# Performance work log

Measured on AMD Instinct MI355X. Metric: run time of the kernel, lower is better.

Reference implementation:

```python
import jax, jax.numpy as jnp
import numpy as np

NEG_INF = -9e15
ALPHA = 0.2  # leaky_relu slope


def gat_layer(h, adj, e_feat, W, We, a_s, a_d, a_e, h_res):
    """Dense multi-head GAT layer with edge features.
    h: [B,N,Fin], adj: [B,N,N] (0/1), e_feat: [B,N,N,Ein]
    W: [H,Fin,Fout], We: [H,Ein,Eout], a_s/a_d: [H,Fout], a_e: [H,Eout]
    Returns head-averaged (x_prime [B,N,Fout], e_prime [B,N,N,Eout]).
    """
    Wh = jnp.einsum('bnf,hfo->bhno', h, W)            # [B,H,N,Fout]
    Me = jnp.einsum('bnmf,hfe->bhnme', e_feat, We)    # [B,H,N,N,Eout]
    s_src = jnp.einsum('bhno,ho->bhn', Wh, a_s)
    s_dst = jnp.einsum('bhno,ho->bhn', Wh, a_d)
    s_edge = jnp.einsum('bhnme,he->bhnm', Me, a_e)
    scores = jax.nn.leaky_relu(s_src[:, :, :, None] + s_dst[:, :, None, :] + s_edge, ALPHA)
    scores = jnp.where(adj[:, None, :, :] > 0, scores, NEG_INF)
    att = jax.nn.softmax(scores, axis=-1)             # [B,H,N,N]
    h_prime = jnp.einsum('bhnm,bhmo->bhno', att, Wh)
    h_prime = jax.nn.elu(h_prime) + h_res[:, None]    # concat=True -> elu; residual add
    e_prime = att[..., None] * Me                      # attention-modulated edge features
    return h_prime.mean(axis=1), e_prime.mean(axis=1)


def setup_inputs() -> dict:
    key = jax.random.key(0)
    ks = jax.random.split(key, 16)
    B, N, F, E, H = 2, 256, 768, 7, 2
    nhid, ehid = 768, 768 // 2
    sc = lambda fan: 1.0 / np.sqrt(fan)
    return {
        'x': jax.random.normal(ks[0], (B, N, F), jnp.float32),
        'adj': jax.random.randint(ks[1], (B, N, N), 0, 2, jnp.int32),
        'e': jax.random.uniform(ks[2], (B, N, N, E), jnp.float32),
        'W1': jax.random.normal(ks[3], (H, F, nhid), jnp.float32) * sc(F),
        'We1': jax.random.normal(ks[4], (H, E, ehid), jnp.float32) * sc(E),
        'a1s': jax.random.normal(ks[5], (H, nhid), jnp.float32) * sc(nhid),
        'a1d': jax.random.normal(ks[6], (H, nhid), jnp.float32) * sc(nhid),
        'a1e': jax.random.normal(ks[7], (H, ehid), jnp.float32) * sc(ehid),
        'W2': jax.random.normal(ks[8], (H, nhid, nhid), jnp.float32) * sc(nhid),
        'We2': jax.random.normal(ks[9], (H, ehid, ehid), jnp.float32) * sc(ehid),
        'a2s': jax.random.normal(ks[10], (H, nhid), jnp.float32) * sc(nhid),
        'a2d': jax.random.normal(ks[11], (H, nhid), jnp.float32) * sc(nhid),
        'a2e': jax.random.normal(ks[12], (H, ehid), jnp.float32) * sc(ehid),
    }


def reference(x, adj, e, W1, We1, a1s, a1d, a1e, W2, We2, a2s, a2d, a2e):
    # dropout layers are identity in eval mode
    x1, e1 = gat_layer(x, adj, e, W1, We1, a1s, a1d, a1e, x)
    x2, e2 = gat_layer(x1, adj, e1, W2, We2, a2s, a2d, a2e, x)
    return x2, e2
```

## Files before the change

kernel.cpp:

```cpp
#include <hip/hip_runtime.h>
#include <hip/hip_bf16.h>
#include <cstddef>


typedef __attribute__((ext_vector_type(8))) short bf16x8;
typedef __attribute__((ext_vector_type(4))) short bf16x4;
typedef __attribute__((ext_vector_type(4))) float f32x4;
typedef unsigned short us;

#define DEVINL static __device__ __forceinline__

DEVINL us f2bf(float f) {
    union { float f; unsigned u; } v; v.f = f;
    return (us)((v.u + 0x7FFFu + ((v.u >> 16) & 1u)) >> 16);
}
DEVINL float bf2f(us b) {
    union { unsigned u; float f; } v; v.u = ((unsigned)b) << 16; return v.f;
}
DEVINL float wredmax(float v) {
#pragma unroll
    for (int s = 32; s; s >>= 1) v = fmaxf(v, __shfl_xor(v, s));
    return v;
}
DEVINL float wredsum(float v) {
#pragma unroll
    for (int s = 32; s; s >>= 1) v += __shfl_xor(v, s);
    return v;
}

DEVINL void transpose_body(const float* __restrict__ W, us* __restrict__ WT, int bb) {
    __shared__ us tile[64][65];
    const int ft = (bb % 12) * 64, ot = ((bb / 12) % 12) * 64, h = bb / 144;
    const int t = threadIdx.x;
    const float* Wh = W + (size_t)h * 768 * 768;
    us* WTh = WT + (size_t)h * 768 * 768;
#pragma unroll
    for (int i = 0; i < 16; i++) {
        int idx = t + i * 256, r = idx >> 6, c = idx & 63;
        tile[c][r] = f2bf(Wh[(ft + r) * 768 + ot + c]);
    }
    __syncthreads();
#pragma unroll
    for (int i = 0; i < 2; i++) {
        int idx = t + i * 256, r = idx >> 3, c0 = (idx & 7) * 8;
        us pk[8];
#pragma unroll
        for (int j = 0; j < 8; j++) pk[j] = tile[r][c0 + j];
        *(bf16x8*)&WTh[(ot + r) * 768 + ft + c0] = *(bf16x8*)pk;
    }
}

DEVINL void cvt_body(const float* __restrict__ in, us* __restrict__ out, int blk) {
    int i = (blk * 256 + threadIdx.x) * 8;
    float4 v0 = *(const float4*)&in[i];
    float4 v1 = *(const float4*)&in[i + 4];
    us pk[8] = {f2bf(v0.x), f2bf(v0.y), f2bf(v0.z), f2bf(v0.w),
                f2bf(v1.x), f2bf(v1.y), f2bf(v1.z), f2bf(v1.w)};
    *(bf16x8*)&out[i] = *(bf16x8*)pk;
}

DEVINL void pre_body(const float* __restrict__ W1, const float* __restrict__ W2,
                     const float* __restrict__ We1, const float* __restrict__ We2,
                     const float* __restrict__ a1s, const float* __restrict__ a1d,
                     const float* __restrict__ a1e, const float* __restrict__ a2s,
                     const float* __restrict__ a2d,
                     float* __restrict__ q, float* __restrict__ u1,
                     float* __restrict__ Mcat, int blk) {
    const int g = blk * 32 + (threadIdx.x >> 3);
    const int lane = threadIdx.x & 7;
    float acc = 0.0f;
    if (g < 6144) {
        int vec = g / 1536, rem = g % 1536, h = rem / 768, f = rem % 768;
        const float* W = (vec < 2) ? W1 : W2;
        const float* a = (vec == 0) ? a1s : (vec == 1) ? a1d : (vec == 2) ? a2s : a2d;
        const float* wr = W + (size_t)(h * 768 + f) * 768;
        const float* ar = a + h * 768;
        for (int o = lane; o < 768; o += 8) acc += wr[o] * ar[o];
        for (int s = 4; s; s >>= 1) acc += __shfl_down(acc, s, 8);
        if (lane == 0) q[g] = acc;
    } else if (g < 6160) {
        int g2 = g - 6144, h = g2 >> 3, k = g2 & 7;
        if (k < 7) {
            const float* wr = We1 + (h * 7 + k) * 384;
            const float* ar = a1e + h * 384;
            for (int o = lane; o < 384; o += 8) acc += wr[o] * ar[o];
        }
        for (int s = 4; s; s >>= 1) acc += __shfl_down(acc, s, 8);
        if (lane == 0) u1[g2] = acc;
    } else if (g < 18448) {
        int g3 = g - 6160, rk = g3 / 384, tc = g3 % 384;
        int hh = rk >> 3, kk = rk & 7, h1 = hh >> 1, h2 = hh & 1;
        if (kk < 7) {
            const float* wr = We1 + (h1 * 7 + kk) * 384;
            const float* w2c = We2 + (size_t)h2 * 384 * 384 + tc;
            for (int o = lane; o < 384; o += 8) acc += wr[o] * w2c[o * 384];
            acc *= 0.25f;
        }
        for (int s = 4; s; s >>= 1) acc += __shfl_down(acc, s, 8);
        if (lane == 0) Mcat[g3] = acc;
    }
}

DEVINL void wcalc_body(const float* __restrict__ Mcat, const float* __restrict__ a2e,
                       float* __restrict__ w) {
    const int t = threadIdx.x, g = t >> 3, lane = t & 7;
    int hh = g >> 3, k = g & 7, h2 = hh & 1;
    float acc = 0.0f;
    if (k < 7)
        for (int o = lane; o < 384; o += 8) acc += Mcat[(hh * 8 + k) * 384 + o] * a2e[h2 * 384 + o];
    for (int s = 4; s; s >>= 1) acc += __shfl_down(acc, s, 8);
    if (lane == 0) w[g] = 2.0f * acc;
}

DEVINL void bfrag_body(const float* __restrict__ Mcat, us* __restrict__ Bfrag, int ct) {
    const int l = threadIdx.x;
    if (l < 64) {
        us pk[8];
#pragma unroll
        for (int j = 0; j < 8; j++)
            pk[j] = f2bf(Mcat[((l >> 4) * 8 + j) * 384 + ct * 16 + (l & 15)]);
        *(bf16x8*)&Bfrag[(ct * 64 + l) * 8] = *(bf16x8*)pk;
    }
}

DEVINL void sdots_body(const float* __restrict__ x, const float* __restrict__ qs,
                       const float* __restrict__ qd, float* __restrict__ out_s,
                       float* __restrict__ out_d, int n, int b) {
    const int t = threadIdx.x, wv = t >> 6;
    const float* xr = x + (size_t)(b * 256 + n) * 768;
    float a0 = 0, a1 = 0, a2 = 0, a3 = 0;
#pragma unroll
    for (int i = 0; i < 3; i++) {
        int k = i * 256 + t;
        float xv = xr[k];
        a0 += xv * qs[k];
        a1 += xv * qs[768 + k];
        a2 += xv * qd[k];
        a3 += xv * qd[768 + k];
    }
    a0 = wredsum(a0); a1 = wredsum(a1); a2 = wredsum(a2); a3 = wredsum(a3);
    __shared__ float part[4][4];
    if ((t & 63) == 0) { part[wv][0] = a0; part[wv][1] = a1; part[wv][2] = a2; part[wv][3] = a3; }
    __syncthreads();
    if (t == 0) {
        float r0 = 0, r1 = 0, r2 = 0, r3 = 0;
#pragma unroll
        for (int i = 0; i < 4; i++) { r0 += part[i][0]; r1 += part[i][1]; r2 += part[i][2]; r3 += part[i][3]; }
        out_s[(b * 2 + 0) * 256 + n] = r0;
        out_s[(b * 2 + 1) * 256 + n] = r1;
        out_d[(b * 2 + 0) * 256 + n] = r2;
        out_d[(b * 2 + 1) * 256 + n] = r3;
    }
}

DEVINL void att_finish2(float sc0, float sc1, us* __restrict__ attb,
                        size_t base0, size_t base1) {
    const int t = threadIdx.x, wv = t >> 6;
    __shared__ float smax[2][4], ssum[2][4];
    float w0 = wredmax(sc0), w1 = wredmax(sc1);
    if ((t & 63) == 0) { smax[0][wv] = w0; smax[1][wv] = w1; }
    __syncthreads();
    float mx0 = fmaxf(fmaxf(smax[0][0], smax[0][1]), fmaxf(smax[0][2], smax[0][3]));
    float mx1 = fmaxf(fmaxf(smax[1][0], smax[1][1]), fmaxf(smax[1][2], smax[1][3]));
    float ex0 = __expf(sc0 - mx0), ex1 = __expf(sc1 - mx1);
    float su0 = wredsum(ex0), su1 = wredsum(ex1);
    if ((t & 63) == 0) { ssum[0][wv] = su0; ssum[1][wv] = su1; }
    __syncthreads();
    float i0 = 1.0f / (ssum[0][0] + ssum[0][1] + ssum[0][2] + ssum[0][3]);
    float i1 = 1.0f / (ssum[1][0] + ssum[1][1] + ssum[1][2] + ssum[1][3]);
    attb[base0 + t] = f2bf(ex0 * i0);
    attb[base1 + t] = f2bf(ex1 * i1);
}

DEVINL void att1_body(const float* __restrict__ e, const int* __restrict__ adj,
                      const float* __restrict__ s_s, const float* __restrict__ s_d,
                      const float* __restrict__ u1, us* __restrict__ attb,
                      int n, int bb) {
    __shared__ float eL[1792];
    const int t = threadIdx.x;
    const float* erow = e + (size_t)(bb * 256 + n) * 256 * 7;
#pragma unroll
    for (int i = 0; i < 7; i++) eL[t + i * 256] = erow[t + i * 256];
    __syncthreads();
    float ss0 = s_s[(bb * 2 + 0) * 256 + n], ss1 = s_s[(bb * 2 + 1) * 256 + n];
    float sd0 = s_d[(bb * 2 + 0) * 256 + t], sd1 = s_d[(bb * 2 + 1) * 256 + t];
    float se0 = 0, se1 = 0;
#pragma unroll
    for (int k = 0; k < 7; k++) {
        float ev = eL[t * 7 + k];
        se0 += ev * u1[k];
        se1 += ev * u1[8 + k];
    }
    float sc0 = ss0 + sd0 + se0, sc1 = ss1 + sd1 + se1;
    sc0 = sc0 > 0.0f ? sc0 : 0.2f * sc0;
    sc1 = sc1 > 0.0f ? sc1 : 0.2f * sc1;
    bool ok = adj[(size_t)(bb * 256 + n) * 256 + t] > 0;
    sc0 = ok ? sc0 : -9e15f;
    sc1 = ok ? sc1 : -9e15f;
    size_t base0 = ((size_t)(bb * 2 + 0) * 256 + n) * 256;
    size_t base1 = ((size_t)(bb * 2 + 1) * 256 + n) * 256;
    att_finish2(sc0, sc1, attb, base0, base1);
}

DEVINL void att2_body(const float* __restrict__ e, const int* __restrict__ adj,
                      const float* __restrict__ s_s, const float* __restrict__ s_d,
                      const float* __restrict__ w, const us* __restrict__ att1b,
                      us* __restrict__ attb, int n, int bb) {
    __shared__ float eL[1792];
    const int t = threadIdx.x;
    const float* erow = e + (size_t)(bb * 256 + n) * 256 * 7;
#pragma unroll
    for (int i = 0; i < 7; i++) eL[t + i * 256] = erow[t + i * 256];
    __syncthreads();
    float ss0 = s_s[(bb * 2 + 0) * 256 + n], ss1 = s_s[(bb * 2 + 1) * 256 + n];
    float sd0 = s_d[(bb * 2 + 0) * 256 + t], sd1 = s_d[(bb * 2 + 1) * 256 + t];
    float a10 = bf2f(att1b[((size_t)(bb * 2 + 0) * 256 + n) * 256 + t]);
    float a11 = bf2f(att1b[((size_t)(bb * 2 + 1) * 256 + n) * 256 + t]);
    float ew00 = 0, ew01 = 0, ew10 = 0, ew11 = 0;
#pragma unroll
    for (int k = 0; k < 7; k++) {
        float ev = eL[t * 7 + k];
        ew00 += ev * w[0 * 8 + k];
        ew01 += ev * w[1 * 8 + k];
        ew10 += ev * w[2 * 8 + k];
        ew11 += ev * w[3 * 8 + k];
    }
    float sc0 = ss0 + sd0 + a10 * ew00 + a11 * ew10;
    float sc1 = ss1 + sd1 + a10 * ew01 + a11 * ew11;
    sc0 = sc0 > 0.0f ? sc0 : 0.2f * sc0;
    sc1 = sc1 > 0.0f ? sc1 : 0.2f * sc1;
    bool ok = adj[(size_t)(bb * 256 + n) * 256 + t] > 0;
    sc0 = ok ? sc0 : -9e15f;
    sc1 = ok ? sc1 : -9e15f;
    size_t base0 = ((size_t)(bb * 2 + 0) * 256 + n) * 256;
    size_t base1 = ((size_t)(bb * 2 + 1) * 256 + n) * 256;
    att_finish2(sc0, sc1, attb, base0, base1);
}

DEVINL void gemm_xw_body(const us* __restrict__ A, const us* __restrict__ BT,
                         us* __restrict__ WhT, int mt, int ot, int h) {
    const int t = threadIdx.x, wv = t >> 6, l = t & 63;
    const int wm = wv >> 1, wn = wv & 1, lr = l & 15, lk = l >> 4;
    __shared__ us As[64][40];
    __shared__ us Bs[64][40];
    const int arow = t >> 2, acol = (t & 3) * 8;
    const us* Bh = BT + (size_t)h * 768 * 768;
    f32x4 acc[2][2];
#pragma unroll
    for (int i = 0; i < 2; i++)
#pragma unroll
        for (int j = 0; j < 2; j++) acc[i][j] = (f32x4){0, 0, 0, 0};
    for (int k0 = 0; k0 < 768; k0 += 32) {
        __syncthreads();
        *(bf16x8*)&As[arow][acol] = *(const bf16x8*)&A[(size_t)(mt * 64 + arow) * 768 + k0 + acol];
        *(bf16x8*)&Bs[arow][acol] = *(const bf16x8*)&Bh[(size_t)(ot * 64 + arow) * 768 + k0 + acol];
        __syncthreads();
        bf16x8 af[2], bfv[2];
#pragma unroll
        for (int i = 0; i < 2; i++) af[i] = *(const bf16x8*)&As[wm * 32 + i * 16 + lr][lk * 8];
#pragma unroll
        for (int j = 0; j < 2; j++) bfv[j] = *(const bf16x8*)&Bs[wn * 32 + j * 16 + lr][lk * 8];
#pragma unroll
        for (int i = 0; i < 2; i++)
#pragma unroll
            for (int j = 0; j < 2; j++)
                acc[i][j] = __builtin_amdgcn_mfma_f32_16x16x32_bf16(af[i], bfv[j], acc[i][j], 0, 0, 0);
    }
#pragma unroll
    for (int i = 0; i < 2; i++)
#pragma unroll
        for (int j = 0; j < 2; j++) {
            int n0 = mt * 64 + wm * 32 + i * 16 + lk * 4;
            int og = ot * 64 + wn * 32 + j * 16 + lr;
            int b = n0 >> 8, n = n0 & 255;
            us pk[4];
#pragma unroll
            for (int r = 0; r < 4; r++) pk[r] = f2bf(acc[i][j][r]);
            *(bf16x4*)&WhT[((size_t)(b * 2 + h) * 768 + og) * 256 + n] = *(bf16x4*)pk;
        }
}

DEVINL void gemm_att_body(const us* __restrict__ attb, const us* __restrict__ WhT,
                          const float* __restrict__ resid, float* __restrict__ xout,
                          us* __restrict__ xbout, int mt, int ot, int b) {
    const int t = threadIdx.x, wv = t >> 6, l = t & 63;
    const int wm = wv >> 1, wn = wv & 1, lr = l & 15, lk = l >> 4;
    __shared__ us As2[32][40];
    __shared__ us Bs2[64][40];
    float res[2][4] = {};
    for (int h = 0; h < 2; h++) {
        const us* Ah = attb + (size_t)(b * 2 + h) * 65536;
        const us* Bh = WhT + (size_t)(b * 2 + h) * 768 * 256;
        f32x4 acc[2];
        acc[0] = (f32x4){0, 0, 0, 0};
        acc[1] = (f32x4){0, 0, 0, 0};
        for (int k0 = 0; k0 < 256; k0 += 32) {
            __syncthreads();
            if (t < 128) {
                int ar = t >> 2, ac = (t & 3) * 8;
                *(bf16x8*)&As2[ar][ac] = *(const bf16x8*)&Ah[(size_t)(mt * 32 + ar) * 256 + k0 + ac];
            }
            {
                int br = t >> 2, bc = (t & 3) * 8;
                *(bf16x8*)&Bs2[br][bc] = *(const bf16x8*)&Bh[(size_t)(ot * 64 + br) * 256 + k0 + bc];
            }
            __syncthreads();
            bf16x8 af = *(const bf16x8*)&As2[wm * 16 + lr][lk * 8];
#pragma unroll
            for (int j = 0; j < 2; j++) {
                bf16x8 bv = *(const bf16x8*)&Bs2[wn * 32 + j * 16 + lr][lk * 8];
                acc[j] = __builtin_amdgcn_mfma_f32_16x16x32_bf16(af, bv, acc[j], 0, 0, 0);
            }
        }
#pragma unroll
        for (int j = 0; j < 2; j++)
#pragma unroll
            for (int r = 0; r < 4; r++) {
                float v = acc[j][r];
                res[j][r] += (v > 0.0f ? v : (expf(v) - 1.0f));
            }
        __syncthreads();
    }
#pragma unroll
    for (int j = 0; j < 2; j++) {
        int n0 = mt * 32 + wm * 16 + lk * 4;
        int og = ot * 64 + wn * 32 + j * 16 + lr;
#pragma unroll
        for (int r = 0; r < 4; r++) {
            size_t idx = (size_t)(b * 256 + n0 + r) * 768 + og;
            float v = 0.5f * res[j][r] + resid[idx];
            xout[idx] = v;
            if (xbout) xbout[idx] = f2bf(v);
        }
    }
}

DEVINL void e2row_body(const float* __restrict__ e, const us* __restrict__ att1b,
                       const us* __restrict__ att2b, const us* __restrict__ Bfrag,
                       float* __restrict__ e2out, int bb, int n) {
    __shared__ us blB[1536 * 8];
    __shared__ float eL[1792];
    __shared__ float aL[4][256];
    const int t = threadIdx.x;
    for (int i = t; i < 1536; i += 256)
        *(bf16x8*)&blB[i * 8] = *(const bf16x8*)&Bfrag[(size_t)i * 8];
    const float* erow = e + (size_t)(bb * 256 + n) * 256 * 7;
#pragma unroll
    for (int i = 0; i < 7; i++) eL[t + i * 256] = erow[t + i * 256];
    const size_t abase = (size_t)bb * 2 * 65536 + n * 256;
    aL[0][t] = bf2f(att1b[abase + t]);
    aL[1][t] = bf2f(att1b[abase + 65536 + t]);
    aL[2][t] = bf2f(att2b[abase + t]);
    aL[3][t] = bf2f(att2b[abase + 65536 + t]);
    __syncthreads();
    const int wv = t >> 6, l = t & 63, le = l & 15, lq = l >> 4;
    const int h1 = lq >> 1, h2 = lq & 1;
    bf16x8 av[4];
#pragma unroll
    for (int g = 0; g < 4; g++) {
        int m = g * 64 + wv * 16 + le;
        float c = aL[h1][m] * aL[2 + h2][m];
        us pk[8];
#pragma unroll
        for (int j = 0; j < 7; j++) pk[j] = f2bf(c * eL[m * 7 + j]);
        pk[7] = 0;
        av[g] = *(bf16x8*)pk;
    }
    const f32x4 zero = {0, 0, 0, 0};
    const size_t rowbase = (size_t)bb * 65536 + n * 256;
#pragma unroll
    for (int cg = 0; cg < 3; cg++) {
        bf16x8 bfr[8];
#pragma unroll
        for (int i = 0; i < 8; i++) bfr[i] = *(const bf16x8*)&blB[(cg * 512 + i * 64 + l) * 8];
        for (int g = 0; g < 4; g++) {
            size_t eidx = rowbase + g * 64 + wv * 16 + le;
#pragma unroll
            for (int i = 0; i < 8; i++) {
                f32x4 acc = __builtin_amdgcn_mfma_f32_16x16x32_bf16(bfr[i], av[g], zero, 0, 0, 0);
                *(f32x4*)&e2out[eidx * 384 + cg * 128 + i * 16 + lq * 4] = acc;
            }
        }
    }
}

__global__ __launch_bounds__(256) void stage1(
    const float* W1, const float* W2, const float* We1, const float* We2,
    const float* a1s, const float* a1d, const float* a1e,
    const float* a2s, const float* a2d,
    const float* x, us* W1T, us* W2T, us* xb,
    float* q, float* u1, float* Mcat) {
    int b = blockIdx.x;
    if (b < 577)       pre_body(W1, W2, We1, We2, a1s, a1d, a1e, a2s, a2d, q, u1, Mcat, b);
    else if (b < 865)  transpose_body(W1, W1T, b - 577);
    else if (b < 1153) transpose_body(W2, W2T, b - 865);
    else               cvt_body(x, xb, b - 1153);
}

__global__ __launch_bounds__(256) void stage2(
    const float* Mcat, const float* a2e, float* wbuf, us* Bfrag,
    const float* x, const float* qs, const float* qd, float* s1s, float* s1d) {
    int b = blockIdx.x;
    if (b < 1)        wcalc_body(Mcat, a2e, wbuf);
    else if (b < 25)  bfrag_body(Mcat, Bfrag, b - 1);
    else { int i = b - 25; sdots_body(x, qs, qd, s1s, s1d, i & 255, i >> 8); }
}

__global__ __launch_bounds__(256) void stage3(
    const float* e, const int* adj, const float* s1s, const float* s1d,
    const float* u1, us* att1b, const us* xb, const us* W1T, us* WhT1) {
    int b = blockIdx.x;
    if (b < 512) att1_body(e, adj, s1s, s1d, u1, att1b, b & 255, b >> 8);
    else { int g = b - 512; gemm_xw_body(xb, W1T, WhT1, g & 7, (g >> 3) % 12, g / 96); }
}

__global__ __launch_bounds__(256) void stage4(
    const us* att1b, const us* WhT1, const float* x, float* x1, us* xb1) {
    int b = blockIdx.x;
    gemm_att_body(att1b, WhT1, x, x1, xb1, b & 7, (b >> 3) % 12, b / 96);
}

__global__ __launch_bounds__(256) void stage5(
    const float* x1, const float* qs, const float* qd, float* s2s, float* s2d,
    const us* xb1, const us* W2T, us* WhT2) {
    int b = blockIdx.x;
    if (b < 512) sdots_body(x1, qs, qd, s2s, s2d, b & 255, b >> 8);
    else { int g = b - 512; gemm_xw_body(xb1, W2T, WhT2, g & 7, (g >> 3) % 12, g / 96); }
}

__global__ __launch_bounds__(256) void stage6(
    const float* e, const int* adj, const float* s2s, const float* s2d,
    const float* wbuf, const us* att1b, us* att2b) {
    int b = blockIdx.x;
    att2_body(e, adj, s2s, s2d, wbuf, att1b, att2b, b & 255, b >> 8);
}

__global__ __launch_bounds__(256) void stage7(
    const us* att2b, const us* WhT2, const float* x, float* x2out,
    const float* e, const us* att1b, const us* Bfrag, float* e2out) {
    int b = blockIdx.x;
    if (b < 192) gemm_att_body(att2b, WhT2, x, x2out, (us*)nullptr, b & 7, (b >> 3) % 12, b / 96);
    else { int r = b - 192; e2row_body(e, att1b, att2b, Bfrag, e2out, r >> 8, r & 255); }
}

extern "C" void kernel_launch(void* const* d_in, const int* in_sizes, int n_in,
                              void* d_out, int out_size, void* d_ws, size_t ws_size,
                              hipStream_t stream) {
    const float* x   = (const float*)d_in[0];
    const int*   adj = (const int*)d_in[1];
    const float* e   = (const float*)d_in[2];
    const float* W1  = (const float*)d_in[3];
    const float* We1 = (const float*)d_in[4];
    const float* a1s = (const float*)d_in[5];
    const float* a1d = (const float*)d_in[6];
    const float* a1e = (const float*)d_in[7];
    const float* W2  = (const float*)d_in[8];
    const float* We2 = (const float*)d_in[9];
    const float* a2s = (const float*)d_in[10];
    const float* a2d = (const float*)d_in[11];
    const float* a2e = (const float*)d_in[12];

    float* out   = (float*)d_out;
    float* x2out = out;
    float* e2out = out + 393216;

    char* ws = (char*)d_ws;
    float* q     = (float*)(ws + 0);
    float* u1    = (float*)(ws + 24576);
    float* wbuf  = (float*)(ws + 24640);
    float* Mcat  = (float*)(ws + 24832);
    us*    Bfrag = (us*)(ws + 73984);
    float* s1s   = (float*)(ws + 98560);
    float* s1d   = (float*)(ws + 102656);
    float* s2s   = (float*)(ws + 106752);
    float* s2d   = (float*)(ws + 110848);
    us*    att1b = (us*)(ws + 114944);
    us*    att2b = (us*)(ws + 639232);
    us*    W1T   = (us*)(ws + 1163520);
    us*    W2T   = (us*)(ws + 3522816);
    us*    xb    = (us*)(ws + 5882112);
    us*    xb1   = (us*)(ws + 6668544);
    us*    WhT1  = (us*)(ws + 7454976);
    us*    WhT2  = (us*)(ws + 9027840);
    float* x1    = (float*)(ws + 10600704);

    stage1<<<1345, 256, 0, stream>>>(W1, W2, We1, We2, a1s, a1d, a1e, a2s, a2d,
                                     x, W1T, W2T, xb, q, u1, Mcat);
    stage2<<<537, 256, 0, stream>>>(Mcat, a2e, wbuf, Bfrag, x, q + 0, q + 1536, s1s, s1d);
    stage3<<<704, 256, 0, stream>>>(e, adj, s1s, s1d, u1, att1b, xb, W1T, WhT1);
    stage4<<<192, 256, 0, stream>>>(att1b, WhT1, x, x1, xb1);
    stage5<<<704, 256, 0, stream>>>(x1, q + 3072, q + 4608, s2s, s2d, xb1, W2T, WhT2);
    stage6<<<512, 256, 0, stream>>>(e, adj, s2s, s2d, wbuf, att1b, att2b);
    stage7<<<704, 256, 0, stream>>>(att2b, WhT2, x, x2out, e, att1b, Bfrag, e2out);
}
```

Baseline: 106.0 us.

## Fuse score dots into GEMM epilogues and merge attention-2 with edge output

The q vectors (W·a) are now computed inside the W transpose blocks using wave reductions and atomics, replacing the separate pre_body pass. The second layer's source and destination score dots are accumulated in the stage4 GEMM epilogue through shared and global atomics, so the x1 fp32 buffer and the sdots stage go away. Attention-2 softmax is fused with the e2 output computation in one block, and Mcat gets a shared-memory tiled kernel. Together these cut the launch count from 7 to 6 and remove extra passes over memory, at the cost of atomics, two memsets, and a summation order that is no longer deterministic.

```diff
diff --git a/kernel.cpp b/kernel.cpp
--- a/kernel.cpp
+++ b/kernel.cpp
@@ -28,16 +28,27 @@
     return v;
 }
 
-DEVINL void transpose_body(const float* __restrict__ W, us* __restrict__ WT, int bb) {
+DEVINL void transposeq_body(const float* __restrict__ W, us* __restrict__ WT,
+                            const float* __restrict__ as_, const float* __restrict__ ad_,
+                            float* __restrict__ q, int qbase, int bb) {
     __shared__ us tile[64][65];
     const int ft = (bb % 12) * 64, ot = ((bb / 12) % 12) * 64, h = bb / 144;
-    const int t = threadIdx.x;
-    const float* Wh = W + (size_t)h * 768 * 768;
-    us* WTh = WT + (size_t)h * 768 * 768;
+    const int t = threadIdx.x, c = t & 63, g = t >> 6;
+    const float* Wh = W + (size_t)h * 589824;
+    us* WTh = WT + (size_t)h * 589824;
+    const float avs = as_[h * 768 + ot + c];
+    const float avd = ad_[h * 768 + ot + c];
 #pragma unroll
     for (int i = 0; i < 16; i++) {
-        int idx = t + i * 256, r = idx >> 6, c = idx & 63;
-        tile[c][r] = f2bf(Wh[(ft + r) * 768 + ot + c]);
+        int r = g + i * 4;
+        float w = Wh[(size_t)(ft + r) * 768 + ot + c];
+        tile[c][r] = f2bf(w);
+        float ss = wredsum(w * avs);
+        float sd = wredsum(w * avd);
+        if (c == 0) {
+            atomicAdd(&q[qbase + h * 768 + ft + r], ss);
+            atomicAdd(&q[qbase + 1536 + h * 768 + ft + r], sd);
+        }
     }
     __syncthreads();
 #pragma unroll
@@ -46,7 +57,56 @@
         us pk[8];
 #pragma unroll
         for (int j = 0; j < 8; j++) pk[j] = tile[r][c0 + j];
-        *(bf16x8*)&WTh[(ot + r) * 768 + ft + c0] = *(bf16x8*)pk;
+        *(bf16x8*)&WTh[(size_t)(ot + r) * 768 + ft + c0] = *(bf16x8*)pk;
+    }
+}
+
+DEVINL void mcat_body(const float* __restrict__ We1, const float* __restrict__ We2,
+                      float* __restrict__ Mcat, int h2, int tct) {
+    __shared__ float we1L[16][384];
+    __shared__ float part[16][128];
+    const int t = threadIdx.x;
+    for (int i = t; i < 6144; i += 256) {
+        int m = i / 384, o = i % 384;
+        int h1 = m >> 3, kk = m & 7;
+        we1L[m][o] = (kk < 7) ? We1[(h1 * 7 + kk) * 384 + o] : 0.0f;
+    }
+    __syncthreads();
+    const int tc = tct * 128 + (t & 127);
+    const int half = t >> 7;
+    float acc[16];
+#pragma unroll
+    for (int m = 0; m < 16; m++) acc[m] = 0.0f;
+    const float* w2 = We2 + (size_t)h2 * 147456 + tc;
+    for (int o = half * 192; o < half * 192 + 192; o++) {
+        float wv = w2[(size_t)o * 384];
+#pragma unroll
+        for (int m = 0; m < 16; m++) acc[m] += we1L[m][o] * wv;
+    }
+    if (half == 1)
+#pragma unroll
+        for (int m = 0; m < 16; m++) part[m][t & 127] = acc[m];
+    __syncthreads();
+    if (half == 0) {
+#pragma unroll
+        for (int m = 0; m < 16; m++) {
+            float v = 0.25f * (acc[m] + part[m][t]);
+            int h1 = m >> 3, kk = m & 7;
+            Mcat[((h1 * 2 + h2) * 8 + kk) * 384 + tc] = v;
+        }
+    }
+}
+
+DEVINL void u1_body(const float* __restrict__ We1, const float* __restrict__ a1e,
+                    float* __restrict__ u1) {
+    const int t = threadIdx.x, g = t >> 4, lane = t & 15;
+    if (g < 14) {
+        int h = g / 7, k = g % 7;
+        float acc = 0.0f;
+        for (int o = lane; o < 384; o += 16) acc += We1[(h * 7 + k) * 384 + o] * a1e[h * 384 + o];
+#pragma unroll
+        for (int s = 8; s; s >>= 1) acc += __shfl_xor(acc, s, 16);
+        if (lane == 0) u1[h * 8 + k] = acc;
     }
 }
 
@@ -57,48 +117,6 @@
     us pk[8] = {f2bf(v0.x), f2bf(v0.y), f2bf(v0.z), f2bf(v0.w),
                 f2bf(v1.x), f2bf(v1.y), f2bf(v1.z), f2bf(v1.w)};
     *(bf16x8*)&out[i] = *(bf16x8*)pk;
-}
-
-DEVINL void pre_body(const float* __restrict__ W1, const float* __restrict__ W2,
-                     const float* __restrict__ We1, const float* __restrict__ We2,
-                     const float* __restrict__ a1s, const float* __restrict__ a1d,
-                     const float* __restrict__ a1e, const float* __restrict__ a2s,
-                     const float* __restrict__ a2d,
-                     float* __restrict__ q, float* __restrict__ u1,
-                     float* __restrict__ Mcat, int blk) {
-    const int g = blk * 32 + (threadIdx.x >> 3);
-    const int lane = threadIdx.x & 7;
-    float acc = 0.0f;
-    if (g < 6144) {
-        int vec = g / 1536, rem = g % 1536, h = rem / 768, f = rem % 768;
-        const float* W = (vec < 2) ? W1 : W2;
-        const float* a = (vec == 0) ? a1s : (vec == 1) ? a1d : (vec == 2) ? a2s : a2d;
-        const float* wr = W + (size_t)(h * 768 + f) * 768;
-        const float* ar = a + h * 768;
-        for (int o = lane; o < 768; o += 8) acc += wr[o] * ar[o];
-        for (int s = 4; s; s >>= 1) acc += __shfl_down(acc, s, 8);
-        if (lane == 0) q[g] = acc;
-    } else if (g < 6160) {
-        int g2 = g - 6144, h = g2 >> 3, k = g2 & 7;
-        if (k < 7) {
-            const float* wr = We1 + (h * 7 + k) * 384;
-            const float* ar = a1e + h * 384;
-            for (int o = lane; o < 384; o += 8) acc += wr[o] * ar[o];
-        }
-        for (int s = 4; s; s >>= 1) acc += __shfl_down(acc, s, 8);
-        if (lane == 0) u1[g2] = acc;
-    } else if (g < 18448) {
-        int g3 = g - 6160, rk = g3 / 384, tc = g3 % 384;
-        int hh = rk >> 3, kk = rk & 7, h1 = hh >> 1, h2 = hh & 1;
-        if (kk < 7) {
-            const float* wr = We1 + (h1 * 7 + kk) * 384;
-            const float* w2c = We2 + (size_t)h2 * 384 * 384 + tc;
-            for (int o = lane; o < 384; o += 8) acc += wr[o] * w2c[o * 384];
-            acc *= 0.25f;
-        }
-        for (int s = 4; s; s >>= 1) acc += __shfl_down(acc, s, 8);
-        if (lane == 0) Mcat[g3] = acc;
-    }
 }
 
 DEVINL void wcalc_body(const float* __restrict__ Mcat, const float* __restrict__ a2e,
@@ -153,32 +171,14 @@
     }
 }
 
-DEVINL void att_finish2(float sc0, float sc1, us* __restrict__ attb,
-                        size_t base0, size_t base1) {
-    const int t = threadIdx.x, wv = t >> 6;
-    __shared__ float smax[2][4], ssum[2][4];
-    float w0 = wredmax(sc0), w1 = wredmax(sc1);
-    if ((t & 63) == 0) { smax[0][wv] = w0; smax[1][wv] = w1; }
-    __syncthreads();
-    float mx0 = fmaxf(fmaxf(smax[0][0], smax[0][1]), fmaxf(smax[0][2], smax[0][3]));
-    float mx1 = fmaxf(fmaxf(smax[1][0], smax[1][1]), fmaxf(smax[1][2], smax[1][3]));
-    float ex0 = __expf(sc0 - mx0), ex1 = __expf(sc1 - mx1);
-    float su0 = wredsum(ex0), su1 = wredsum(ex1);
-    if ((t & 63) == 0) { ssum[0][wv] = su0; ssum[1][wv] = su1; }
-    __syncthreads();
-    float i0 = 1.0f / (ssum[0][0] + ssum[0][1] + ssum[0][2] + ssum[0][3]);
-    float i1 = 1.0f / (ssum[1][0] + ssum[1][1] + ssum[1][2] + ssum[1][3]);
-    attb[base0 + t] = f2bf(ex0 * i0);
-    attb[base1 + t] = f2bf(ex1 * i1);
-}
-
 DEVINL void att1_body(const float* __restrict__ e, const int* __restrict__ adj,
                       const float* __restrict__ s_s, const float* __restrict__ s_d,
                       const float* __restrict__ u1, us* __restrict__ attb,
                       int n, int bb) {
     __shared__ float eL[1792];
-    const int t = threadIdx.x;
-    const float* erow = e + (size_t)(bb * 256 + n) * 256 * 7;
+    __shared__ float smax[2][4], ssum[2][4];
+    const int t = threadIdx.x, wv = t >> 6;
+    const float* erow = e + (size_t)(bb * 256 + n) * 1792;
 #pragma unroll
     for (int i = 0; i < 7; i++) eL[t + i * 256] = erow[t + i * 256];
     __syncthreads();
@@ -197,44 +197,19 @@
     bool ok = adj[(size_t)(bb * 256 + n) * 256 + t] > 0;
     sc0 = ok ? sc0 : -9e15f;
     sc1 = ok ? sc1 : -9e15f;
-    size_t base0 = ((size_t)(bb * 2 + 0) * 256 + n) * 256;
-    size_t base1 = ((size_t)(bb * 2 + 1) * 256 + n) * 256;
-    att_finish2(sc0, sc1, attb, base0, base1);
-}
-
-DEVINL void att2_body(const float* __restrict__ e, const int* __restrict__ adj,
-                      const float* __restrict__ s_s, const float* __restrict__ s_d,
-                      const float* __restrict__ w, const us* __restrict__ att1b,
-                      us* __restrict__ attb, int n, int bb) {
-    __shared__ float eL[1792];
-    const int t = threadIdx.x;
-    const float* erow = e + (size_t)(bb * 256 + n) * 256 * 7;
-#pragma unroll
-    for (int i = 0; i < 7; i++) eL[t + i * 256] = erow[t + i * 256];
-    __syncthreads();
-    float ss0 = s_s[(bb * 2 + 0) * 256 + n], ss1 = s_s[(bb * 2 + 1) * 256 + n];
-    float sd0 = s_d[(bb * 2 + 0) * 256 + t], sd1 = s_d[(bb * 2 + 1) * 256 + t];
-    float a10 = bf2f(att1b[((size_t)(bb * 2 + 0) * 256 + n) * 256 + t]);
-    float a11 = bf2f(att1b[((size_t)(bb * 2 + 1) * 256 + n) * 256 + t]);
-    float ew00 = 0, ew01 = 0, ew10 = 0, ew11 = 0;
-#pragma unroll
-    for (int k = 0; k < 7; k++) {
-        float ev = eL[t * 7 + k];
-        ew00 += ev * w[0 * 8 + k];
-        ew01 += ev * w[1 * 8 + k];
-        ew10 += ev * w[2 * 8 + k];
-        ew11 += ev * w[3 * 8 + k];
-    }
-    float sc0 = ss0 + sd0 + a10 * ew00 + a11 * ew10;
-    float sc1 = ss1 + sd1 + a10 * ew01 + a11 * ew11;
-    sc0 = sc0 > 0.0f ? sc0 : 0.2f * sc0;
-    sc1 = sc1 > 0.0f ? sc1 : 0.2f * sc1;
-    bool ok = adj[(size_t)(bb * 256 + n) * 256 + t] > 0;
-    sc0 = ok ? sc0 : -9e15f;
-    sc1 = ok ? sc1 : -9e15f;
-    size_t base0 = ((size_t)(bb * 2 + 0) * 256 + n) * 256;
-    size_t base1 = ((size_t)(bb * 2 + 1) * 256 + n) * 256;
-    att_finish2(sc0, sc1, attb, base0, base1);
+    float w0 = wredmax(sc0), w1 = wredmax(sc1);
+    if ((t & 63) == 0) { smax[0][wv] = w0; smax[1][wv] = w1; }
+    __syncthreads();
+    float mx0 = fmaxf(fmaxf(smax[0][0], smax[0][1]), fmaxf(smax[0][2], smax[0][3]));
+    float mx1 = fmaxf(fmaxf(smax[1][0], smax[1][1]), fmaxf(smax[1][2], smax[1][3]));
+    float ex0 = __expf(sc0 - mx0), ex1 = __expf(sc1 - mx1);
+    float su0 = wredsum(ex0), su1 = wredsum(ex1);
+    if ((t & 63) == 0) { ssum[0][wv] = su0; ssum[1][wv] = su1; }
+    __syncthreads();
+    float i0 = 1.0f / (ssum[0][0] + ssum[0][1] + ssum[0][2] + ssum[0][3]);
+    float i1 = 1.0f / (ssum[1][0] + ssum[1][1] + ssum[1][2] + ssum[1][3]);
+    attb[((size_t)(bb * 2 + 0) * 256 + n) * 256 + t] = f2bf(ex0 * i0);
+    attb[((size_t)(bb * 2 + 1) * 256 + n) * 256 + t] = f2bf(ex1 * i1);
 }
 
 DEVINL void gemm_xw_body(const us* __restrict__ A, const us* __restrict__ BT,
@@ -244,7 +219,7 @@
     __shared__ us As[64][40];
     __shared__ us Bs[64][40];
     const int arow = t >> 2, acol = (t & 3) * 8;
-    const us* Bh = BT + (size_t)h * 768 * 768;
+    const us* Bh = BT + (size_t)h * 589824;
     f32x4 acc[2][2];
 #pragma unroll
     for (int i = 0; i < 2; i++)
@@ -282,15 +257,19 @@
 
 DEVINL void gemm_att_body(const us* __restrict__ attb, const us* __restrict__ WhT,
                           const float* __restrict__ resid, float* __restrict__ xout,
-                          us* __restrict__ xbout, int mt, int ot, int b) {
+                          us* __restrict__ xbout, const float* __restrict__ q,
+                          float* __restrict__ s2s, float* __restrict__ s2d,
+                          int mt, int ot, int b) {
     const int t = threadIdx.x, wv = t >> 6, l = t & 63;
     const int wm = wv >> 1, wn = wv & 1, lr = l & 15, lk = l >> 4;
     __shared__ us As2[32][40];
     __shared__ us Bs2[64][40];
+    __shared__ float sAcc[4][32];
+    if (s2s && t < 128) ((float*)sAcc)[t] = 0.0f;
     float res[2][4] = {};
     for (int h = 0; h < 2; h++) {
         const us* Ah = attb + (size_t)(b * 2 + h) * 65536;
-        const us* Bh = WhT + (size_t)(b * 2 + h) * 768 * 256;
+        const us* Bh = WhT + (size_t)(b * 2 + h) * 196608;
         f32x4 acc[2];
         acc[0] = (f32x4){0, 0, 0, 0};
         acc[1] = (f32x4){0, 0, 0, 0};
@@ -325,33 +304,94 @@
     for (int j = 0; j < 2; j++) {
         int n0 = mt * 32 + wm * 16 + lk * 4;
         int og = ot * 64 + wn * 32 + j * 16 + lr;
+        float qs0 = 0, qs1 = 0, qd0 = 0, qd1 = 0;
+        if (s2s) {
+            qs0 = q[3072 + og]; qs1 = q[3072 + 768 + og];
+            qd0 = q[4608 + og]; qd1 = q[4608 + 768 + og];
+        }
 #pragma unroll
         for (int r = 0; r < 4; r++) {
             size_t idx = (size_t)(b * 256 + n0 + r) * 768 + og;
             float v = 0.5f * res[j][r] + resid[idx];
-            xout[idx] = v;
+            if (xout) xout[idx] = v;
             if (xbout) xbout[idx] = f2bf(v);
-        }
-    }
-}
-
-DEVINL void e2row_body(const float* __restrict__ e, const us* __restrict__ att1b,
-                       const us* __restrict__ att2b, const us* __restrict__ Bfrag,
-                       float* __restrict__ e2out, int bb, int n) {
+            if (s2s) {
+                int row = wm * 16 + lk * 4 + r;
+                atomicAdd(&sAcc[0][row], v * qs0);
+                atomicAdd(&sAcc[1][row], v * qs1);
+                atomicAdd(&sAcc[2][row], v * qd0);
+                atomicAdd(&sAcc[3][row], v * qd1);
+            }
+        }
+    }
+    if (s2s) {
+        __syncthreads();
+        if (t < 128) {
+            int type = t >> 5, row = t & 31, n = mt * 32 + row;
+            float* dst = (type == 0) ? &s2s[(b * 2 + 0) * 256 + n]
+                       : (type == 1) ? &s2s[(b * 2 + 1) * 256 + n]
+                       : (type == 2) ? &s2d[(b * 2 + 0) * 256 + n]
+                                     : &s2d[(b * 2 + 1) * 256 + n];
+            atomicAdd(dst, sAcc[type][row]);
+        }
+    }
+}
+
+DEVINL void att2e2_body(const float* __restrict__ e, const int* __restrict__ adj,
+                        const float* __restrict__ s_s, const float* __restrict__ s_d,
+                        const float* __restrict__ w, const us* __restrict__ att1b,
+                        us* __restrict__ att2b, const us* __restrict__ Bfrag,
+                        float* __restrict__ e2out, int bb, int n) {
     __shared__ us blB[1536 * 8];
     __shared__ float eL[1792];
-    __shared__ float aL[4][256];
-    const int t = threadIdx.x;
+    __shared__ float aL1[2][256], aL2[2][256];
+    __shared__ float smax[2][4], ssum[2][4];
+    const int t = threadIdx.x, wv4 = t >> 6;
     for (int i = t; i < 1536; i += 256)
         *(bf16x8*)&blB[i * 8] = *(const bf16x8*)&Bfrag[(size_t)i * 8];
-    const float* erow = e + (size_t)(bb * 256 + n) * 256 * 7;
+    const float* erow = e + (size_t)(bb * 256 + n) * 1792;
 #pragma unroll
     for (int i = 0; i < 7; i++) eL[t + i * 256] = erow[t + i * 256];
-    const size_t abase = (size_t)bb * 2 * 65536 + n * 256;
-    aL[0][t] = bf2f(att1b[abase + t]);
-    aL[1][t] = bf2f(att1b[abase + 65536 + t]);
-    aL[2][t] = bf2f(att2b[abase + t]);
-    aL[3][t] = bf2f(att2b[abase + 65536 + t]);
+    const size_t a1base = (size_t)bb * 131072 + n * 256;
+    float a10 = bf2f(att1b[a1base + t]);
+    float a11 = bf2f(att1b[a1base + 65536 + t]);
+    aL1[0][t] = a10;
+    aL1[1][t] = a11;
+    __syncthreads();
+    float ss0 = s_s[(bb * 2 + 0) * 256 + n], ss1 = s_s[(bb * 2 + 1) * 256 + n];
+    float sd0 = s_d[(bb * 2 + 0) * 256 + t], sd1 = s_d[(bb * 2 + 1) * 256 + t];
+    float ew00 = 0, ew01 = 0, ew10 = 0, ew11 = 0;
+#pragma unroll
+    for (int k = 0; k < 7; k++) {
+        float ev = eL[t * 7 + k];
+        ew00 += ev * w[k];
+        ew01 += ev * w[8 + k];
+        ew10 += ev * w[16 + k];
+        ew11 += ev * w[24 + k];
+    }
+    float sc0 = ss0 + sd0 + a10 * ew00 + a11 * ew10;
+    float sc1 = ss1 + sd1 + a10 * ew01 + a11 * ew11;
+    sc0 = sc0 > 0.0f ? sc0 : 0.2f * sc0;
+    sc1 = sc1 > 0.0f ? sc1 : 0.2f * sc1;
+    bool ok = adj[(size_t)(bb * 256 + n) * 256 + t] > 0;
+    sc0 = ok ? sc0 : -9e15f;
+    sc1 = ok ? sc1 : -9e15f;
+    float w0 = wredmax(sc0), w1 = wredmax(sc1);
+    if ((t & 63) == 0) { smax[0][wv4] = w0; smax[1][wv4] = w1; }
+    __syncthreads();
+    float mx0 = fmaxf(fmaxf(smax[0][0], smax[0][1]), fmaxf(smax[0][2], smax[0][3]));
+    float mx1 = fmaxf(fmaxf(smax[1][0], smax[1][1]), fmaxf(smax[1][2], smax[1][3]));
+    float ex0 = __expf(sc0 - mx0), ex1 = __expf(sc1 - mx1);
+    float su0 = wredsum(ex0), su1 = wredsum(ex1);
+    if ((t & 63) == 0) { ssum[0][wv4] = su0; ssum[1][wv4] = su1; }
+    __syncthreads();
+    float i0 = 1.0f / (ssum[0][0] + ssum[0][1] + ssum[0][2] + ssum[0][3]);
+    float i1 = 1.0f / (ssum[1][0] + ssum[1][1] + ssum[1][2] + ssum[1][3]);
+    float v0 = ex0 * i0, v1 = ex1 * i1;
+    att2b[((size_t)(bb * 2 + 0) * 256 + n) * 256 + t] = f2bf(v0);
+    att2b[((size_t)(bb * 2 + 1) * 256 + n) * 256 + t] = f2bf(v1);
+    aL2[0][t] = v0;
+    aL2[1][t] = v1;
     __syncthreads();
     const int wv = t >> 6, l = t & 63, le = l & 15, lq = l >> 4;
     const int h1 = lq >> 1, h2 = lq & 1;
@@ -359,7 +399,7 @@
 #pragma unroll
     for (int g = 0; g < 4; g++) {
         int m = g * 64 + wv * 16 + le;
-        float c = aL[h1][m] * aL[2 + h2][m];
+        float c = aL1[h1][m] * aL2[h2][m];
         us pk[8];
 #pragma unroll
         for (int j = 0; j < 7; j++) pk[j] = f2bf(c * eL[m * 7 + j]);
@@ -387,14 +427,14 @@
 __global__ __launch_bounds__(256) void stage1(
     const float* W1, const float* W2, const float* We1, const float* We2,
     const float* a1s, const float* a1d, const float* a1e,
-    const float* a2s, const float* a2d,
-    const float* x, us* W1T, us* W2T, us* xb,
-    float* q, float* u1, float* Mcat) {
+    const float* a2s, const float* a2d, const float* x,
+    us* W1T, us* W2T, us* xb, float* q, float* u1, float* Mcat) {
     int b = blockIdx.x;
-    if (b < 577)       pre_body(W1, W2, We1, We2, a1s, a1d, a1e, a2s, a2d, q, u1, Mcat, b);
-    else if (b < 865)  transpose_body(W1, W1T, b - 577);
-    else if (b < 1153) transpose_body(W2, W2T, b - 865);
-    else               cvt_body(x, xb, b - 1153);
+    if (b < 6)          mcat_body(We1, We2, Mcat, b & 1, b >> 1);
+    else if (b == 6)    u1_body(We1, a1e, u1);
+    else if (b < 295)   transposeq_body(W1, W1T, a1s, a1d, q, 0, b - 7);
+    else if (b < 583)   transposeq_body(W2, W2T, a2s, a2d, q, 3072, b - 295);
+    else                cvt_body(x, xb, b - 583);
 }
 
 __global__ __launch_bounds__(256) void stage2(
@@ -415,32 +455,28 @@
 }
 
 __global__ __launch_bounds__(256) void stage4(
-    const us* att1b, const us* WhT1, const float* x, float* x1, us* xb1) {
+    const us* att1b, const us* WhT1, const float* x, us* xb1,
+    const float* q, float* s2s, float* s2d) {
     int b = blockIdx.x;
-    gemm_att_body(att1b, WhT1, x, x1, xb1, b & 7, (b >> 3) % 12, b / 96);
+    gemm_att_body(att1b, WhT1, x, (float*)nullptr, xb1, q, s2s, s2d,
+                  b & 7, (b >> 3) % 12, b / 96);
 }
 
 __global__ __launch_bounds__(256) void stage5(
-    const float* x1, const float* qs, const float* qd, float* s2s, float* s2d,
+    const float* e, const int* adj, const float* s2s, const float* s2d,
+    const float* wbuf, const us* att1b, us* att2b, const us* Bfrag, float* e2out,
     const us* xb1, const us* W2T, us* WhT2) {
     int b = blockIdx.x;
-    if (b < 512) sdots_body(x1, qs, qd, s2s, s2d, b & 255, b >> 8);
+    if (b < 512) att2e2_body(e, adj, s2s, s2d, wbuf, att1b, att2b, Bfrag, e2out,
+                             b >> 8, b & 255);
     else { int g = b - 512; gemm_xw_body(xb1, W2T, WhT2, g & 7, (g >> 3) % 12, g / 96); }
 }
 
 __global__ __launch_bounds__(256) void stage6(
-    const float* e, const int* adj, const float* s2s, const float* s2d,
-    const float* wbuf, const us* att1b, us* att2b) {
+    const us* att2b, const us* WhT2, const float* x, float* x2out) {
     int b = blockIdx.x;
-    att2_body(e, adj, s2s, s2d, wbuf, att1b, att2b, b & 255, b >> 8);
-}
-
-__global__ __launch_bounds__(256) void stage7(
-    const us* att2b, const us* WhT2, const float* x, float* x2out,
-    const float* e, const us* att1b, const us* Bfrag, float* e2out) {
-    int b = blockIdx.x;
-    if (b < 192) gemm_att_body(att2b, WhT2, x, x2out, (us*)nullptr, b & 7, (b >> 3) % 12, b / 96);
-    else { int r = b - 192; e2row_body(e, att1b, att2b, Bfrag, e2out, r >> 8, r & 255); }
+    gemm_att_body(att2b, WhT2, x, x2out, (us*)nullptr, (const float*)nullptr,
+                  (float*)nullptr, (float*)nullptr, b & 7, (b >> 3) % 12, b / 96);
 }
 
 extern "C" void kernel_launch(void* const* d_in, const int* in_sizes, int n_in,
@@ -482,14 +518,16 @@
     us*    xb1   = (us*)(ws + 6668544);
     us*    WhT1  = (us*)(ws + 7454976);
     us*    WhT2  = (us*)(ws + 9027840);
-    float* x1    = (float*)(ws + 10600704);
-
-    stage1<<<1345, 256, 0, stream>>>(W1, W2, We1, We2, a1s, a1d, a1e, a2s, a2d,
-                                     x, W1T, W2T, xb, q, u1, Mcat);
+
+    hipMemsetAsync(q, 0, 24576, stream);
+    hipMemsetAsync(s2s, 0, 8192, stream);
+
+    stage1<<<775, 256, 0, stream>>>(W1, W2, We1, We2, a1s, a1d, a1e, a2s, a2d,
+                                    x, W1T, W2T, xb, q, u1, Mcat);
     stage2<<<537, 256, 0, stream>>>(Mcat, a2e, wbuf, Bfrag, x, q + 0, q + 1536, s1s, s1d);
     stage3<<<704, 256, 0, stream>>>(e, adj, s1s, s1d, u1, att1b, xb, W1T, WhT1);
-    stage4<<<192, 256, 0, stream>>>(att1b, WhT1, x, x1, xb1);
-    stage5<<<704, 256, 0, stream>>>(x1, q + 3072, q + 4608, s2s, s2d, xb1, W2T, WhT2);
-    stage6<<<512, 256, 0, stream>>>(e, adj, s2s, s2d, wbuf, att1b, att2b);
-    stage7<<<704, 256, 0, stream>>>(att2b, WhT2, x, x2out, e, att1b, Bfrag, e2out);
-}
+    stage4<<<192, 256, 0, stream>>>(att1b, WhT1, x, xb1, q, s2s, s2d);
+    stage5<<<704, 256, 0, stream>>>(e, adj, s2s, s2d, wbuf, att1b, att2b, Bfrag, e2out,
+                                    xb1, W2T, WhT2);
+    stage6<<<192, 256, 0, stream>>>(att2b, WhT2, x, x2out);
+}
```

New measurement: 145.9 us. 1.38x slower.
